# Optimization experiments

Hardware: AMD Instinct MI355X
Metric: run time of the kernel (lower is better)

## Reference

```python
import jax, jax.numpy as jnp
import numpy as np

BLOCK = 64
KH = 8        # num_k_head
G = 4         # gqa_group_size
D = 128       # model_hidden_size (head dim)
DG = 128      # gate_hidden_size
EPS = 1e-6
BSZ = 4
MAXS = 4096
LENGTHS = np.array([4096, 3584, 3072, 4096])


def rotate_half(x):
    h = x.shape[-1] // 2
    return jnp.concatenate([-x[..., h:], x[..., :h]], axis=-1)


def rmsnorm(x, w):
    x32 = x.astype(jnp.float32)
    y = x32 * jax.lax.rsqrt(jnp.mean(x32 * x32, axis=-1, keepdims=True) + EPS)
    return (y * w).astype(x.dtype)


def _rope_tables(n_pos, dim):
    inv = 1.0 / (10000.0 ** (np.arange(0, dim, 2, dtype=np.float32) / dim))
    ang = np.arange(n_pos, dtype=np.float32)[:, None] * inv[None, :]
    emb = np.concatenate([ang, ang], axis=-1)
    return np.cos(emb), np.sin(emb)


def setup_inputs() -> dict:
    key = jax.random.key(0)
    k1, k2, k3, k4, k5, k6 = jax.random.split(key, 6)
    total = int(LENGTHS.sum())
    cu = np.concatenate([[0], np.cumsum(LENGTHS)]).astype(np.int32)
    unpad_idx = np.concatenate([b * MAXS + np.arange(L) for b, L in enumerate(LENGTHS)]).astype(np.int64)
    # block-causal + validity mask (bool), shape (BSZ, 1, MAXS, MAXS//BLOCK)
    nb = MAXS // BLOCK
    qpos = np.arange(MAXS)
    bidx = np.arange(nb)
    causal = (qpos[:, None] // BLOCK) >= bidx[None, :]
    qvalid = qpos[None, :] < LENGTHS[:, None]
    bvalid = (bidx * BLOCK)[None, :] < LENGTHS[:, None]
    mask = causal[None] & qvalid[:, :, None] & bvalid[:, None, :]
    cos_q, sin_q = _rope_tables(MAXS, DG)
    cos_k, sin_k = _rope_tables(nb, DG)
    xavq = float(np.sqrt(6.0 / (D + DG)))
    xavk = float(np.sqrt(6.0 / (2 * D + DG)))
    return {
        "q": jax.random.normal(k1, (total, KH * G, D), jnp.float32),
        "k": jax.random.normal(k2, (total, KH, D), jnp.float32),
        "wq": jax.random.uniform(k3, (KH, G, D, DG), jnp.float32, -xavq, xavq),
        "wk": jax.random.uniform(k4, (KH, 2 * D, DG), jnp.float32, -xavk, xavk),
        "qnorm_w": jnp.ones((DG,), jnp.float32),
        "knorm_w": jnp.ones((DG,), jnp.float32),
        "cos_q": jnp.tile(jnp.asarray(cos_q)[None], (BSZ, 1, 1)),
        "sin_q": jnp.tile(jnp.asarray(sin_q)[None], (BSZ, 1, 1)),
        "cos_k": jnp.tile(jnp.asarray(cos_k)[None], (BSZ, 1, 1)),
        "sin_k": jnp.tile(jnp.asarray(sin_k)[None], (BSZ, 1, 1)),
        "attention_mask": jnp.asarray(mask)[:, None, :, :],
        "cu_seqlens": jnp.asarray(cu),
        "unpad_indices": jnp.asarray(unpad_idx),
        "max_seqlen": MAXS,
    }


def reference(q, k, wq, wk, qnorm_w, knorm_w, cos_q, sin_q, cos_k, sin_k,
              attention_mask, cu_seqlens, unpad_indices, max_seqlen):
    T = q.shape[0]
    bsz = cu_seqlens.shape[0] - 1
    nb = max_seqlen // BLOCK
    lengths = cu_seqlens[1:] - cu_seqlens[:-1]

    # --- Q path: per-group head-pooling projection (HeadPoolingLinear, Qproj) ---
    qp = jnp.einsum('skgi,kgio->sko', q.reshape(T, KH, G, D), wq)  # (T, KH, DG)
    qpad = jnp.zeros((bsz * max_seqlen, KH, DG), q.dtype).at[unpad_indices].set(qp)
    qpad = qpad.reshape(bsz, max_seqlen, KH, DG).transpose(0, 2, 1, 3)  # (b, KH, S, DG)
    qpad = rmsnorm(qpad, qnorm_w)
    qpad = qpad * cos_q[:, None] + rotate_half(qpad) * sin_q[:, None]

    # --- K path: pad, block max+avg pool (masked for varlen), project ---
    kpad = jnp.zeros((bsz * max_seqlen, KH, D), k.dtype).at[unpad_indices].set(k)
    kpad = kpad.reshape(bsz, nb, BLOCK, KH, D)
    pos = jnp.arange(max_seqlen).reshape(nb, BLOCK)
    valid = pos[None] < lengths[:, None, None]          # (b, nb, BLOCK)
    v = valid[..., None, None]                          # (b, nb, BLOCK, 1, 1)
    cnt = valid.sum(-1)[..., None, None]                # (b, nb, 1, 1)
    kmax = jnp.where(v, kpad, -jnp.inf).max(axis=2)
    kmax = jnp.where(cnt > 0, kmax, 0.0)
    kavg = jnp.where(v, kpad, 0.0).sum(axis=2) / jnp.maximum(cnt, 1).astype(k.dtype)
    kcat = jnp.concatenate([kmax, kavg], axis=-1)       # (b, nb, KH, 2D)
    kk = jnp.einsum('bhsi,hio->bhso', kcat.transpose(0, 2, 1, 3), wk)  # (b, KH, nb, DG)
    kk = rmsnorm(kk, knorm_w)
    kk = kk * cos_k[:, None] + rotate_half(kk) * sin_k[:, None]

    # --- QK gate scores ---
    attn = jnp.einsum('bhsd,bhtd->bhst', qpad, kk) * (1.0 / np.sqrt(DG))
    return jnp.where(attention_mask, attn, -1e20)
```

## Files before the change

### kernel.cpp

```cpp
#include <hip/hip_runtime.h>
#include <cstdint>
#include <cstddef>

#define BSZ   4
#define MAXS  4096
#define NB    64
#define KH    8
#define GQ    4
#define DH    128
#define DG    128
#define KHGD  4096
#define GD    512

__global__ __launch_bounds__(256, 2)
void qproj_kernel(const float* __restrict__ q,
                  const float* __restrict__ wq,
                  const float* __restrict__ qnw,
                  const float* __restrict__ cosq,
                  const float* __restrict__ sinq,
                  const int*   __restrict__ cu,
                  float* __restrict__ qr,
                  int T)
{
    __shared__ float At[64][68];
    __shared__ float Bt[64][128];

    const int tid = threadIdx.x;
    const int h   = blockIdx.y;
    const int t0  = blockIdx.x * 64;
    const int tr  = tid >> 4;
    const int tc  = tid & 15;

    float acc[4][8];
#pragma unroll
    for (int j = 0; j < 4; ++j)
#pragma unroll
        for (int i = 0; i < 8; ++i) acc[j][i] = 0.f;

    const float* qb = q  + (size_t)t0 * KHGD + (size_t)h * GD;
    const float* wb = wq + (size_t)h * GD * DG;

    const float* Ar  = &At[tr * 4][0];
    const float* Bp0 = &Bt[0][tc * 4];
    const float* Bp1 = &Bt[0][64 + tc * 4];

    for (int kc = 0; kc < 8; ++kc) {
        const int kb = kc * 64;
#pragma unroll
        for (int i = 0; i < 4; ++i) {
            const int fid = tid + i * 256;
            const int m = fid >> 4, c4 = (fid & 15) * 4;
            const int mg = (t0 + m < T) ? m : 0;
            const float4 v = *(const float4*)(qb + (size_t)mg * KHGD + kb + c4);
            *(float4*)&At[m][c4] = v;
        }
#pragma unroll
        for (int i = 0; i < 8; ++i) {
            const int fid = tid + i * 256;
            const int kk = fid >> 5, o4 = (fid & 31) * 4;
            const float4 v = *(const float4*)(wb + (size_t)(kb + kk) * DG + o4);
            *(float4*)&Bt[kk][o4] = v;
        }
        __syncthreads();

#pragma unroll 8
        for (int kk = 0; kk < 64; ++kk) {
            const float a0 = Ar[kk];
            const float a1 = Ar[68 + kk];
            const float a2 = Ar[136 + kk];
            const float a3 = Ar[204 + kk];
            const float4 b0 = *(const float4*)(Bp0 + kk * 128);
            const float4 b1 = *(const float4*)(Bp1 + kk * 128);
#define QROW(j, aj)                                                         \
            acc[j][0] += aj * b0.x; acc[j][1] += aj * b0.y;                 \
            acc[j][2] += aj * b0.z; acc[j][3] += aj * b0.w;                 \
            acc[j][4] += aj * b1.x; acc[j][5] += aj * b1.y;                 \
            acc[j][6] += aj * b1.z; acc[j][7] += aj * b1.w;
            QROW(0, a0) QROW(1, a1) QROW(2, a2) QROW(3, a3)
#undef QROW
        }
        __syncthreads();
    }

    const int cu1 = cu[1], cu2 = cu[2], cu3 = cu[3];
    const float4 w0 = *(const float4*)(qnw + tc * 4);
    const float4 w1 = *(const float4*)(qnw + 64 + tc * 4);

#pragma unroll
    for (int j = 0; j < 4; ++j) {
        const int t = t0 + tr * 4 + j;
        float ss = 0.f;
#pragma unroll
        for (int i = 0; i < 8; ++i) ss += acc[j][i] * acc[j][i];
        ss += __shfl_xor(ss, 1);
        ss += __shfl_xor(ss, 2);
        ss += __shfl_xor(ss, 4);
        ss += __shfl_xor(ss, 8);
        const float r = 1.0f / sqrtf(ss * (1.0f / 128.0f) + 1e-6f);

        if (t < T) {
            int b = 0;
            if (t >= cu1) b = 1;
            if (t >= cu2) b = 2;
            if (t >= cu3) b = 3;
            const int cub = (b == 0) ? 0 : ((b == 1) ? cu1 : ((b == 2) ? cu2 : cu3));
            const int s = t - cub;

            float y[8];
            y[0] = acc[j][0] * r * w0.x; y[1] = acc[j][1] * r * w0.y;
            y[2] = acc[j][2] * r * w0.z; y[3] = acc[j][3] * r * w0.w;
            y[4] = acc[j][4] * r * w1.x; y[5] = acc[j][5] * r * w1.y;
            y[6] = acc[j][6] * r * w1.z; y[7] = acc[j][7] * r * w1.w;

            const float* cb = cosq + ((size_t)b * MAXS + s) * DG;
            const float* sb = sinq + ((size_t)b * MAXS + s) * DG;
            const float4 c0 = *(const float4*)(cb + tc * 4);
            const float4 c1 = *(const float4*)(cb + 64 + tc * 4);
            const float4 s0v = *(const float4*)(sb + tc * 4);
            const float4 s1v = *(const float4*)(sb + 64 + tc * 4);

            float4 o0, o1;
            o0.x = y[0] * c0.x - y[4] * s0v.x;
            o0.y = y[1] * c0.y - y[5] * s0v.y;
            o0.z = y[2] * c0.z - y[6] * s0v.z;
            o0.w = y[3] * c0.w - y[7] * s0v.w;
            o1.x = y[4] * c1.x + y[0] * s1v.x;
            o1.y = y[5] * c1.y + y[1] * s1v.y;
            o1.z = y[6] * c1.z + y[2] * s1v.z;
            o1.w = y[7] * c1.w + y[3] * s1v.w;

            float* qrow = qr + (((size_t)b * KH + h) * MAXS + s) * DG;
            *(float4*)(qrow + tc * 4)      = o0;
            *(float4*)(qrow + 64 + tc * 4) = o1;
        }
    }
}

__global__ __launch_bounds__(256, 2)
void kproj_kernel(const float* __restrict__ k,
                  const float* __restrict__ wk,
                  const float* __restrict__ knw,
                  const float* __restrict__ cosk,
                  const float* __restrict__ sink,
                  const int*   __restrict__ cu,
                  float* __restrict__ krT)
{
    __shared__ float kcat[KH][2 * DH];

    const int tid = threadIdx.x;
    const int blk = blockIdx.x, b = blockIdx.y;
    const int lb = cu[b];
    const int L  = cu[b + 1] - lb;
    const int nv = min(64, L - blk * 64);
    if (nv <= 0) return;

    const float* kbase = k + (size_t)(lb + blk * 64) * (KH * DH) + tid * 4;
    float4 vmax = make_float4(-3.0e38f, -3.0e38f, -3.0e38f, -3.0e38f);
    float4 vsum = make_float4(0.f, 0.f, 0.f, 0.f);
#pragma unroll 4
    for (int j = 0; j < nv; ++j) {
        const float4 v = *(const float4*)(kbase + (size_t)j * (KH * DH));
        vmax.x = fmaxf(vmax.x, v.x); vmax.y = fmaxf(vmax.y, v.y);
        vmax.z = fmaxf(vmax.z, v.z); vmax.w = fmaxf(vmax.w, v.w);
        vsum.x += v.x; vsum.y += v.y; vsum.z += v.z; vsum.w += v.w;
    }
    {
        const float inv = 1.0f / (float)nv;
        const int hh = tid >> 5, dd = (tid & 31) * 4;
        *(float4*)&kcat[hh][dd] = vmax;
        const float4 va = make_float4(vsum.x * inv, vsum.y * inv, vsum.z * inv, vsum.w * inv);
        *(float4*)&kcat[hh][128 + dd] = va;
    }
    __syncthreads();

    const int h = tid >> 5, oc = tid & 31, o = oc * 4;
    float4 a4 = make_float4(0.f, 0.f, 0.f, 0.f);
    const float* wbb = wk + (size_t)h * (2 * DH) * DG + o;
#pragma unroll 8
    for (int kk = 0; kk < 2 * DH; ++kk) {
        const float a = kcat[h][kk];
        const float4 w = *(const float4*)(wbb + (size_t)kk * DG);
        a4.x += a * w.x; a4.y += a * w.y; a4.z += a * w.z; a4.w += a * w.w;
    }

    float ss = a4.x * a4.x + a4.y * a4.y + a4.z * a4.z + a4.w * a4.w;
    ss += __shfl_xor(ss, 1);
    ss += __shfl_xor(ss, 2);
    ss += __shfl_xor(ss, 4);
    ss += __shfl_xor(ss, 8);
    ss += __shfl_xor(ss, 16);
    const float r = 1.0f / sqrtf(ss * (1.0f / 128.0f) + 1e-6f);

    const float4 wn = *(const float4*)(knw + o);
    const float y0 = a4.x * r * wn.x;
    const float y1 = a4.y * r * wn.y;
    const float y2 = a4.z * r * wn.z;
    const float y3 = a4.w * r * wn.w;

    const float p0 = __shfl_xor(y0, 16);
    const float p1 = __shfl_xor(y1, 16);
    const float p2 = __shfl_xor(y2, 16);
    const float p3 = __shfl_xor(y3, 16);
    const float r0 = (oc < 16) ? -p0 : p0;
    const float r1 = (oc < 16) ? -p1 : p1;
    const float r2 = (oc < 16) ? -p2 : p2;
    const float r3 = (oc < 16) ? -p3 : p3;

    const float* cb = cosk + ((size_t)b * NB + blk) * DG + o;
    const float* sb = sink + ((size_t)b * NB + blk) * DG + o;
    const float4 c4 = *(const float4*)cb;
    const float4 s4 = *(const float4*)sb;

    float* ko = krT + (((size_t)b * KH + h) * DG + o) * NB + blk;
    ko[0 * NB] = y0 * c4.x + r0 * s4.x;
    ko[1 * NB] = y1 * c4.y + r1 * s4.y;
    ko[2 * NB] = y2 * c4.z + r2 * s4.z;
    ko[3 * NB] = y3 * c4.w + r3 * s4.w;
}

__global__ __launch_bounds__(256, 2)
void score_kernel(const float* __restrict__ qr,
                  const float* __restrict__ krT,
                  const int*   __restrict__ cu,
                  float* __restrict__ out)
{
    __shared__ float qtT[64][68];
    __shared__ float kt[128][64];

    const int tid = threadIdx.x;
    const int c = blockIdx.x, h = blockIdx.y, b = blockIdx.z;
    const int L  = cu[b + 1] - cu[b];
    const int s0 = c * 64;
    float* ob = out + (((size_t)b * KH + h) * MAXS + s0) * NB;

    if (s0 >= L) {
        const float4 m4 = make_float4(-1e20f, -1e20f, -1e20f, -1e20f);
#pragma unroll
        for (int i = 0; i < 4; ++i)
            *(float4*)(ob + (size_t)(tid + i * 256) * 4) = m4;
        return;
    }
    const int nt = c + 1;

    const float* ktg = krT + ((size_t)b * KH + h) * DG * NB;
#pragma unroll
    for (int i = 0; i < 8; ++i) {
        const int fid = tid + i * 256;
        const int o = fid >> 4, tp = (fid & 15) * 4;
        *(float4*)&kt[o][tp] = *(const float4*)(ktg + (size_t)o * NB + tp);
    }

    const int ts = tid & 15;
    const int tq = tid >> 4;
    float acc[4][4];
#pragma unroll
    for (int j = 0; j < 4; ++j)
#pragma unroll
        for (int i = 0; i < 4; ++i) acc[j][i] = 0.f;

    const float* qg = qr + (((size_t)b * KH + h) * MAXS + s0) * DG;

    for (int ko = 0; ko < 128; ko += 64) {
        __syncthreads();
#pragma unroll
        for (int i = 0; i < 4; ++i) {
            const int fid = tid + i * 256;
            const int m = fid >> 4, c4 = (fid & 15) * 4;
            const float4 v = *(const float4*)(qg + (size_t)m * DG + ko + c4);
            qtT[c4 + 0][m] = v.x;
            qtT[c4 + 1][m] = v.y;
            qtT[c4 + 2][m] = v.z;
            qtT[c4 + 3][m] = v.w;
        }
        __syncthreads();

        if (tq * 4 < nt) {
#pragma unroll 8
            for (int oo = 0; oo < 64; ++oo) {
                const float4 av = *(const float4*)&qtT[oo][ts * 4];
                const float4 bv = *(const float4*)&kt[ko + oo][tq * 4];
                acc[0][0] += av.x * bv.x; acc[0][1] += av.x * bv.y;
                acc[0][2] += av.x * bv.z; acc[0][3] += av.x * bv.w;
                acc[1][0] += av.y * bv.x; acc[1][1] += av.y * bv.y;
                acc[1][2] += av.y * bv.z; acc[1][3] += av.y * bv.w;
                acc[2][0] += av.z * bv.x; acc[2][1] += av.z * bv.y;
                acc[2][2] += av.z * bv.z; acc[2][3] += av.z * bv.w;
                acc[3][0] += av.w * bv.x; acc[3][1] += av.w * bv.y;
                acc[3][2] += av.w * bv.z; acc[3][3] += av.w * bv.w;
            }
        }
    }

    const float scale = 0.08838834764831845f;
#pragma unroll
    for (int j = 0; j < 4; ++j) {
        const int s = s0 + ts * 4 + j;
        const bool sv = (s < L);
        float4 v;
        v.x = (sv && (tq * 4 + 0) < nt) ? acc[j][0] * scale : -1e20f;
        v.y = (sv && (tq * 4 + 1) < nt) ? acc[j][1] * scale : -1e20f;
        v.z = (sv && (tq * 4 + 2) < nt) ? acc[j][2] * scale : -1e20f;
        v.w = (sv && (tq * 4 + 3) < nt) ? acc[j][3] * scale : -1e20f;
        *(float4*)(ob + (size_t)(ts * 4 + j) * NB + tq * 4) = v;
    }
}

extern "C" void kernel_launch(void* const* d_in, const int* in_sizes, int n_in,
                              void* d_out, int out_size, void* d_ws, size_t ws_size,
                              hipStream_t stream)
{
    const float* q    = (const float*)d_in[0];
    const float* k    = (const float*)d_in[1];
    const float* wq   = (const float*)d_in[2];
    const float* wk   = (const float*)d_in[3];
    const float* qnw  = (const float*)d_in[4];
    const float* knw  = (const float*)d_in[5];
    const float* cosq = (const float*)d_in[6];
    const float* sinq = (const float*)d_in[7];
    const float* cosk = (const float*)d_in[8];
    const float* sink = (const float*)d_in[9];
    const int* cu = (const int*)d_in[11];

    const int T = in_sizes[0] / KHGD;

    float* qr  = (float*)d_ws;
    float* krT = qr + (size_t)BSZ * KH * MAXS * DG;
    (void)ws_size; (void)n_in; (void)out_size;

    dim3 g1((T + 63) / 64, KH);
    qproj_kernel<<<g1, 256, 0, stream>>>(q, wq, qnw, cosq, sinq, cu, qr, T);
    kproj_kernel<<<dim3(NB, BSZ), 256, 0, stream>>>(k, wk, knw, cosk, sink, cu, krT);
    score_kernel<<<dim3(NB, KH, BSZ), 256, 0, stream>>>(qr, krT, cu, (float*)d_out);
}
```

Baseline: 588.9 us.

## Use split-bf16 MFMA for Q projection and score GEMMs

Replaces the scalar FP32 FMA GEMMs in the Q projection and score kernels with bf16 MFMA instructions. To keep accuracy close to FP32, each operand is split into hi and lo bf16 parts and three MFMAs are issued per tile. A new prep kernel repacks wq into an MFMA-friendly hi/lo layout on every call. Intermediate Q and K are stored as bf16 hi/lo pairs in an unpadded row layout. The trade-off is three times the matrix-core instructions plus conversion overhead, and some precision risk from dropping the lo*lo term.

Result: faster. 513.7 us (-12.8%).

```diff
diff --git a/kernel.cpp b/kernel.cpp
--- a/kernel.cpp
+++ b/kernel.cpp
@@ -6,132 +6,162 @@
 #define MAXS  4096
 #define NB    64
 #define KH    8
-#define GQ    4
 #define DH    128
 #define DG    128
 #define KHGD  4096
 #define GD    512
 
-__global__ __launch_bounds__(256, 2)
-void qproj_kernel(const float* __restrict__ q,
-                  const float* __restrict__ wq,
-                  const float* __restrict__ qnw,
-                  const float* __restrict__ cosq,
-                  const float* __restrict__ sinq,
-                  const int*   __restrict__ cu,
-                  float* __restrict__ qr,
-                  int T)
-{
-    __shared__ float At[64][68];
-    __shared__ float Bt[64][128];
-
-    const int tid = threadIdx.x;
-    const int h   = blockIdx.y;
-    const int t0  = blockIdx.x * 64;
-    const int tr  = tid >> 4;
-    const int tc  = tid & 15;
-
-    float acc[4][8];
-#pragma unroll
-    for (int j = 0; j < 4; ++j)
-#pragma unroll
-        for (int i = 0; i < 8; ++i) acc[j][i] = 0.f;
-
-    const float* qb = q  + (size_t)t0 * KHGD + (size_t)h * GD;
-    const float* wb = wq + (size_t)h * GD * DG;
-
-    const float* Ar  = &At[tr * 4][0];
-    const float* Bp0 = &Bt[0][tc * 4];
-    const float* Bp1 = &Bt[0][64 + tc * 4];
-
-    for (int kc = 0; kc < 8; ++kc) {
-        const int kb = kc * 64;
-#pragma unroll
-        for (int i = 0; i < 4; ++i) {
-            const int fid = tid + i * 256;
-            const int m = fid >> 4, c4 = (fid & 15) * 4;
-            const int mg = (t0 + m < T) ? m : 0;
-            const float4 v = *(const float4*)(qb + (size_t)mg * KHGD + kb + c4);
-            *(float4*)&At[m][c4] = v;
+typedef __attribute__((ext_vector_type(8))) short  short8;
+typedef __attribute__((ext_vector_type(4))) float  f32x4;
+
+static __device__ __forceinline__ unsigned bf16hi_bits(float x) {
+    unsigned u = __float_as_uint(x);
+    return (u + 0x7FFFu + ((u >> 16) & 1u)) & 0xFFFF0000u;
+}
+static __device__ __forceinline__ unsigned short bf16_rne(float x) {
+    unsigned u = __float_as_uint(x);
+    return (unsigned short)((u + 0x7FFFu + ((u >> 16) & 1u)) >> 16);
+}
+
+__global__ __launch_bounds__(256)
+void prep_wq(const float* __restrict__ wq, unsigned short* __restrict__ Bp)
+{
+    const int wid  = blockIdx.x * 4 + (threadIdx.x >> 6);
+    const int lane = threadIdx.x & 63;
+    const int h  = wid >> 7, kt = (wid >> 4) & 7, kf = (wid >> 3) & 1, cf = wid & 7;
+    const int n  = cf * 16 + (lane & 15);
+    const int k0 = kt * 64 + kf * 32 + (lane >> 4) * 8;
+
+    short8 hi, lo;
+#pragma unroll
+    for (int j = 0; j < 8; ++j) {
+        const float x = wq[(size_t)(h * GD + k0 + j) * DG + n];
+        const unsigned hb = bf16hi_bits(x);
+        hi[j] = (short)(hb >> 16);
+        lo[j] = (short)bf16_rne(x - __uint_as_float(hb));
+    }
+    unsigned short* p = Bp + (size_t)wid * 1024 + lane * 8;
+    *(short8*)p         = hi;
+    *(short8*)(p + 512) = lo;
+}
+
+__global__ __launch_bounds__(64, 2)
+void qproj_mfma(const float* __restrict__ q,
+                const unsigned short* __restrict__ Bp,
+                const float* __restrict__ qnw,
+                const float* __restrict__ cosq,
+                const float* __restrict__ sinq,
+                const int*   __restrict__ cu,
+                unsigned short* __restrict__ qh,
+                unsigned short* __restrict__ ql,
+                int T)
+{
+    const int lane = threadIdx.x;
+    const int h    = blockIdx.x;
+    const int row0 = blockIdx.y * 64;
+    const int lr = lane & 15, lq = lane >> 4;
+
+    f32x4 acc[4][8];
+#pragma unroll
+    for (int rf = 0; rf < 4; ++rf)
+#pragma unroll
+        for (int cf = 0; cf < 8; ++cf) acc[rf][cf] = (f32x4){0.f, 0.f, 0.f, 0.f};
+
+    const float* qb = q + (size_t)h * GD + lq * 8;
+    const float* aptr[4];
+#pragma unroll
+    for (int rf = 0; rf < 4; ++rf) {
+        int grow = row0 + rf * 16 + lr;
+        if (grow > T - 1) grow = T - 1;
+        aptr[rf] = qb + (size_t)grow * KHGD;
+    }
+
+    for (int kt = 0; kt < 8; ++kt) {
+        const int kb = kt * 64;
+#pragma unroll
+        for (int kf = 0; kf < 2; ++kf) {
+            f32x4 a0[4], a1[4];
+#pragma unroll
+            for (int rf = 0; rf < 4; ++rf) {
+                const float* p = aptr[rf] + kb + kf * 32;
+                a0[rf] = *(const f32x4*)p;
+                a1[rf] = *(const f32x4*)(p + 4);
+            }
+            short8 ah[4], al[4];
+#pragma unroll
+            for (int rf = 0; rf < 4; ++rf) {
+#pragma unroll
+                for (int j = 0; j < 4; ++j) {
+                    float x = a0[rf][j];
+                    unsigned hb = bf16hi_bits(x);
+                    ah[rf][j] = (short)(hb >> 16);
+                    al[rf][j] = (short)bf16_rne(x - __uint_as_float(hb));
+                    float y = a1[rf][j];
+                    unsigned hb2 = bf16hi_bits(y);
+                    ah[rf][j + 4] = (short)(hb2 >> 16);
+                    al[rf][j + 4] = (short)bf16_rne(y - __uint_as_float(hb2));
+                }
+            }
+            const unsigned short* bp =
+                Bp + (size_t)(((h * 8 + kt) * 2 + kf) * 8) * 1024 + lane * 8;
+#pragma unroll
+            for (int cf = 0; cf < 8; ++cf) {
+                const short8 bh = *(const short8*)(bp + cf * 1024);
+                const short8 bl = *(const short8*)(bp + cf * 1024 + 512);
+#pragma unroll
+                for (int rf = 0; rf < 4; ++rf) {
+                    acc[rf][cf] = __builtin_amdgcn_mfma_f32_16x16x32_bf16(ah[rf], bh, acc[rf][cf], 0, 0, 0);
+                    acc[rf][cf] = __builtin_amdgcn_mfma_f32_16x16x32_bf16(ah[rf], bl, acc[rf][cf], 0, 0, 0);
+                    acc[rf][cf] = __builtin_amdgcn_mfma_f32_16x16x32_bf16(al[rf], bh, acc[rf][cf], 0, 0, 0);
+                }
+            }
         }
-#pragma unroll
-        for (int i = 0; i < 8; ++i) {
-            const int fid = tid + i * 256;
-            const int kk = fid >> 5, o4 = (fid & 31) * 4;
-            const float4 v = *(const float4*)(wb + (size_t)(kb + kk) * DG + o4);
-            *(float4*)&Bt[kk][o4] = v;
-        }
-        __syncthreads();
-
-#pragma unroll 8
-        for (int kk = 0; kk < 64; ++kk) {
-            const float a0 = Ar[kk];
-            const float a1 = Ar[68 + kk];
-            const float a2 = Ar[136 + kk];
-            const float a3 = Ar[204 + kk];
-            const float4 b0 = *(const float4*)(Bp0 + kk * 128);
-            const float4 b1 = *(const float4*)(Bp1 + kk * 128);
-#define QROW(j, aj)                                                         \
-            acc[j][0] += aj * b0.x; acc[j][1] += aj * b0.y;                 \
-            acc[j][2] += aj * b0.z; acc[j][3] += aj * b0.w;                 \
-            acc[j][4] += aj * b1.x; acc[j][5] += aj * b1.y;                 \
-            acc[j][6] += aj * b1.z; acc[j][7] += aj * b1.w;
-            QROW(0, a0) QROW(1, a1) QROW(2, a2) QROW(3, a3)
-#undef QROW
-        }
-        __syncthreads();
     }
 
     const int cu1 = cu[1], cu2 = cu[2], cu3 = cu[3];
-    const float4 w0 = *(const float4*)(qnw + tc * 4);
-    const float4 w1 = *(const float4*)(qnw + 64 + tc * 4);
-
-#pragma unroll
-    for (int j = 0; j < 4; ++j) {
-        const int t = t0 + tr * 4 + j;
-        float ss = 0.f;
-#pragma unroll
-        for (int i = 0; i < 8; ++i) ss += acc[j][i] * acc[j][i];
-        ss += __shfl_xor(ss, 1);
-        ss += __shfl_xor(ss, 2);
-        ss += __shfl_xor(ss, 4);
-        ss += __shfl_xor(ss, 8);
-        const float r = 1.0f / sqrtf(ss * (1.0f / 128.0f) + 1e-6f);
-
-        if (t < T) {
-            int b = 0;
-            if (t >= cu1) b = 1;
-            if (t >= cu2) b = 2;
-            if (t >= cu3) b = 3;
-            const int cub = (b == 0) ? 0 : ((b == 1) ? cu1 : ((b == 2) ? cu2 : cu3));
-            const int s = t - cub;
-
-            float y[8];
-            y[0] = acc[j][0] * r * w0.x; y[1] = acc[j][1] * r * w0.y;
-            y[2] = acc[j][2] * r * w0.z; y[3] = acc[j][3] * r * w0.w;
-            y[4] = acc[j][4] * r * w1.x; y[5] = acc[j][5] * r * w1.y;
-            y[6] = acc[j][6] * r * w1.z; y[7] = acc[j][7] * r * w1.w;
-
-            const float* cb = cosq + ((size_t)b * MAXS + s) * DG;
-            const float* sb = sinq + ((size_t)b * MAXS + s) * DG;
-            const float4 c0 = *(const float4*)(cb + tc * 4);
-            const float4 c1 = *(const float4*)(cb + 64 + tc * 4);
-            const float4 s0v = *(const float4*)(sb + tc * 4);
-            const float4 s1v = *(const float4*)(sb + 64 + tc * 4);
-
-            float4 o0, o1;
-            o0.x = y[0] * c0.x - y[4] * s0v.x;
-            o0.y = y[1] * c0.y - y[5] * s0v.y;
-            o0.z = y[2] * c0.z - y[6] * s0v.z;
-            o0.w = y[3] * c0.w - y[7] * s0v.w;
-            o1.x = y[4] * c1.x + y[0] * s1v.x;
-            o1.y = y[5] * c1.y + y[1] * s1v.y;
-            o1.z = y[6] * c1.z + y[2] * s1v.z;
-            o1.w = y[7] * c1.w + y[3] * s1v.w;
-
-            float* qrow = qr + (((size_t)b * KH + h) * MAXS + s) * DG;
-            *(float4*)(qrow + tc * 4)      = o0;
-            *(float4*)(qrow + 64 + tc * 4) = o1;
+    float wn[8];
+#pragma unroll
+    for (int cf = 0; cf < 8; ++cf) wn[cf] = qnw[cf * 16 + lr];
+
+#pragma unroll
+    for (int rf = 0; rf < 4; ++rf) {
+#pragma unroll
+        for (int r = 0; r < 4; ++r) {
+            float vv[8];
+            float ss = 0.f;
+#pragma unroll
+            for (int cf = 0; cf < 8; ++cf) { vv[cf] = acc[rf][cf][r]; ss += vv[cf] * vv[cf]; }
+            ss += __shfl_xor(ss, 1);
+            ss += __shfl_xor(ss, 2);
+            ss += __shfl_xor(ss, 4);
+            ss += __shfl_xor(ss, 8);
+            const float rn = 1.0f / sqrtf(ss * (1.0f / 128.0f) + 1e-6f);
+
+            const int t = row0 + rf * 16 + lq * 4 + r;
+            if (t < T) {
+                int b = 0, cub = 0;
+                if (t >= cu1) { b = 1; cub = cu1; }
+                if (t >= cu2) { b = 2; cub = cu2; }
+                if (t >= cu3) { b = 3; cub = cu3; }
+                const int s = t - cub;
+
+                float y[8];
+#pragma unroll
+                for (int cf = 0; cf < 8; ++cf) y[cf] = vv[cf] * rn * wn[cf];
+
+                const float* cb = cosq + ((size_t)b * MAXS + s) * DG + lr;
+                const float* sb = sinq + ((size_t)b * MAXS + s) * DG + lr;
+                unsigned short* oh = qh + ((size_t)t * KH + h) * DG + lr;
+                unsigned short* ol = ql + ((size_t)t * KH + h) * DG + lr;
+#pragma unroll
+                for (int cf = 0; cf < 8; ++cf) {
+                    const float rot = (cf < 4) ? -y[cf + 4] : y[cf - 4];
+                    const float o = y[cf] * cb[cf * 16] + rot * sb[cf * 16];
+                    const unsigned hb = bf16hi_bits(o);
+                    oh[cf * 16] = (unsigned short)(hb >> 16);
+                    ol[cf * 16] = bf16_rne(o - __uint_as_float(hb));
+                }
+            }
         }
     }
 }
@@ -143,7 +173,8 @@
                   const float* __restrict__ cosk,
                   const float* __restrict__ sink,
                   const int*   __restrict__ cu,
-                  float* __restrict__ krT)
+                  unsigned short* __restrict__ krh,
+                  unsigned short* __restrict__ krl)
 {
     __shared__ float kcat[KH][2 * DH];
 
@@ -211,97 +242,86 @@
     const float4 c4 = *(const float4*)cb;
     const float4 s4 = *(const float4*)sb;
 
-    float* ko = krT + (((size_t)b * KH + h) * DG + o) * NB + blk;
-    ko[0 * NB] = y0 * c4.x + r0 * s4.x;
-    ko[1 * NB] = y1 * c4.y + r1 * s4.y;
-    ko[2 * NB] = y2 * c4.z + r2 * s4.z;
-    ko[3 * NB] = y3 * c4.w + r3 * s4.w;
+    float v[4];
+    v[0] = y0 * c4.x + r0 * s4.x;
+    v[1] = y1 * c4.y + r1 * s4.y;
+    v[2] = y2 * c4.z + r2 * s4.z;
+    v[3] = y3 * c4.w + r3 * s4.w;
+
+    ushort4 sh, sl;
+    unsigned hb;
+    hb = bf16hi_bits(v[0]); sh.x = (unsigned short)(hb >> 16); sl.x = bf16_rne(v[0] - __uint_as_float(hb));
+    hb = bf16hi_bits(v[1]); sh.y = (unsigned short)(hb >> 16); sl.y = bf16_rne(v[1] - __uint_as_float(hb));
+    hb = bf16hi_bits(v[2]); sh.z = (unsigned short)(hb >> 16); sl.z = bf16_rne(v[2] - __uint_as_float(hb));
+    hb = bf16hi_bits(v[3]); sh.w = (unsigned short)(hb >> 16); sl.w = bf16_rne(v[3] - __uint_as_float(hb));
+
+    const size_t ko = (((size_t)b * KH + h) * NB + blk) * DG + o;
+    *(ushort4*)(krh + ko) = sh;
+    *(ushort4*)(krl + ko) = sl;
 }
 
 __global__ __launch_bounds__(256, 2)
-void score_kernel(const float* __restrict__ qr,
-                  const float* __restrict__ krT,
-                  const int*   __restrict__ cu,
-                  float* __restrict__ out)
-{
-    __shared__ float qtT[64][68];
-    __shared__ float kt[128][64];
-
+void score_mfma(const unsigned short* __restrict__ qh,
+                const unsigned short* __restrict__ ql,
+                const unsigned short* __restrict__ krh,
+                const unsigned short* __restrict__ krl,
+                const int* __restrict__ cu,
+                float* __restrict__ out, int T)
+{
     const int tid = threadIdx.x;
+    const int lane = tid & 63, wid = tid >> 6;
     const int c = blockIdx.x, h = blockIdx.y, b = blockIdx.z;
-    const int L  = cu[b + 1] - cu[b];
-    const int s0 = c * 64;
-    float* ob = out + (((size_t)b * KH + h) * MAXS + s0) * NB;
-
-    if (s0 >= L) {
-        const float4 m4 = make_float4(-1e20f, -1e20f, -1e20f, -1e20f);
-#pragma unroll
-        for (int i = 0; i < 4; ++i)
-            *(float4*)(ob + (size_t)(tid + i * 256) * 4) = m4;
+    const int L = cu[b + 1] - cu[b];
+    float* ob = out + (((size_t)b * KH + h) * MAXS + c * 64) * NB;
+
+    if (c * 64 >= L) {
+        const f32x4 m4 = (f32x4){-1e20f, -1e20f, -1e20f, -1e20f};
+#pragma unroll
+        for (int i = 0; i < 4; ++i) ((f32x4*)ob)[tid + i * 256] = m4;
         return;
     }
-    const int nt = c + 1;
-
-    const float* ktg = krT + ((size_t)b * KH + h) * DG * NB;
-#pragma unroll
-    for (int i = 0; i < 8; ++i) {
-        const int fid = tid + i * 256;
-        const int o = fid >> 4, tp = (fid & 15) * 4;
-        *(float4*)&kt[o][tp] = *(const float4*)(ktg + (size_t)o * NB + tp);
-    }
-
-    const int ts = tid & 15;
-    const int tq = tid >> 4;
-    float acc[4][4];
-#pragma unroll
-    for (int j = 0; j < 4; ++j)
-#pragma unroll
-        for (int i = 0; i < 4; ++i) acc[j][i] = 0.f;
-
-    const float* qg = qr + (((size_t)b * KH + h) * MAXS + s0) * DG;
-
-    for (int ko = 0; ko < 128; ko += 64) {
-        __syncthreads();
-#pragma unroll
-        for (int i = 0; i < 4; ++i) {
-            const int fid = tid + i * 256;
-            const int m = fid >> 4, c4 = (fid & 15) * 4;
-            const float4 v = *(const float4*)(qg + (size_t)m * DG + ko + c4);
-            qtT[c4 + 0][m] = v.x;
-            qtT[c4 + 1][m] = v.y;
-            qtT[c4 + 2][m] = v.z;
-            qtT[c4 + 3][m] = v.w;
+    const int nt  = c + 1;
+    const int ncf = (nt + 15) >> 4;
+    const int lr = lane & 15, lq = lane >> 4;
+
+    int qrow = cu[b] + c * 64 + wid * 16 + lr;
+    if (qrow > T - 1) qrow = T - 1;
+    const unsigned short* qhp = qh + ((size_t)qrow * KH + h) * DG + lq * 8;
+    const unsigned short* qlp = ql + ((size_t)qrow * KH + h) * DG + lq * 8;
+    const unsigned short* kbh = krh + (((size_t)b * KH + h) * NB + lr) * DG + lq * 8;
+    const unsigned short* kbl = krl + (((size_t)b * KH + h) * NB + lr) * DG + lq * 8;
+
+    f32x4 acc[4];
+#pragma unroll
+    for (int cf = 0; cf < 4; ++cf) acc[cf] = (f32x4){0.f, 0.f, 0.f, 0.f};
+
+#pragma unroll
+    for (int kf = 0; kf < 4; ++kf) {
+        const short8 ah = *(const short8*)(qhp + kf * 32);
+        const short8 al = *(const short8*)(qlp + kf * 32);
+#pragma unroll
+        for (int cf = 0; cf < 4; ++cf) {
+            if (cf < ncf) {
+                const short8 bh = *(const short8*)(kbh + cf * 2048 + kf * 32);
+                const short8 bl = *(const short8*)(kbl + cf * 2048 + kf * 32);
+                acc[cf] = __builtin_amdgcn_mfma_f32_16x16x32_bf16(ah, bh, acc[cf], 0, 0, 0);
+                acc[cf] = __builtin_amdgcn_mfma_f32_16x16x32_bf16(ah, bl, acc[cf], 0, 0, 0);
+                acc[cf] = __builtin_amdgcn_mfma_f32_16x16x32_bf16(al, bh, acc[cf], 0, 0, 0);
+            }
         }
-        __syncthreads();
-
-        if (tq * 4 < nt) {
-#pragma unroll 8
-            for (int oo = 0; oo < 64; ++oo) {
-                const float4 av = *(const float4*)&qtT[oo][ts * 4];
-                const float4 bv = *(const float4*)&kt[ko + oo][tq * 4];
-                acc[0][0] += av.x * bv.x; acc[0][1] += av.x * bv.y;
-                acc[0][2] += av.x * bv.z; acc[0][3] += av.x * bv.w;
-                acc[1][0] += av.y * bv.x; acc[1][1] += av.y * bv.y;
-                acc[1][2] += av.y * bv.z; acc[1][3] += av.y * bv.w;
-                acc[2][0] += av.z * bv.x; acc[2][1] += av.z * bv.y;
-                acc[2][2] += av.z * bv.z; acc[2][3] += av.z * bv.w;
-                acc[3][0] += av.w * bv.x; acc[3][1] += av.w * bv.y;
-                acc[3][2] += av.w * bv.z; acc[3][3] += av.w * bv.w;
-            }
+    }
+
+    const float scale = 0.08838834764831845f;
+#pragma unroll
+    for (int cf = 0; cf < 4; ++cf) {
+        const int t = cf * 16 + lr;
+#pragma unroll
+        for (int r = 0; r < 4; ++r) {
+            const int srow = c * 64 + wid * 16 + lq * 4 + r;
+            float v = (cf < ncf) ? acc[cf][r] * scale : -1e20f;
+            v = (srow < L && t < nt) ? v : -1e20f;
+            ob[(size_t)(wid * 16 + lq * 4 + r) * NB + t] = v;
         }
-    }
-
-    const float scale = 0.08838834764831845f;
-#pragma unroll
-    for (int j = 0; j < 4; ++j) {
-        const int s = s0 + ts * 4 + j;
-        const bool sv = (s < L);
-        float4 v;
-        v.x = (sv && (tq * 4 + 0) < nt) ? acc[j][0] * scale : -1e20f;
-        v.y = (sv && (tq * 4 + 1) < nt) ? acc[j][1] * scale : -1e20f;
-        v.z = (sv && (tq * 4 + 2) < nt) ? acc[j][2] * scale : -1e20f;
-        v.w = (sv && (tq * 4 + 3) < nt) ? acc[j][3] * scale : -1e20f;
-        *(float4*)(ob + (size_t)(ts * 4 + j) * NB + tq * 4) = v;
     }
 }
 
@@ -319,16 +339,19 @@
     const float* sinq = (const float*)d_in[7];
     const float* cosk = (const float*)d_in[8];
     const float* sink = (const float*)d_in[9];
-    const int* cu = (const int*)d_in[11];
+    const int*   cu   = (const int*)d_in[11];
 
     const int T = in_sizes[0] / KHGD;
 
-    float* qr  = (float*)d_ws;
-    float* krT = qr + (size_t)BSZ * KH * MAXS * DG;
+    unsigned short* qh  = (unsigned short*)d_ws;
+    unsigned short* ql  = qh  + (size_t)T * KH * DG;
+    unsigned short* krh = ql  + (size_t)T * KH * DG;
+    unsigned short* krl = krh + (size_t)BSZ * KH * NB * DG;
+    unsigned short* Bp  = krl + (size_t)BSZ * KH * NB * DG;
     (void)ws_size; (void)n_in; (void)out_size;
 
-    dim3 g1((T + 63) / 64, KH);
-    qproj_kernel<<<g1, 256, 0, stream>>>(q, wq, qnw, cosq, sinq, cu, qr, T);
-    kproj_kernel<<<dim3(NB, BSZ), 256, 0, stream>>>(k, wk, knw, cosk, sink, cu, krT);
-    score_kernel<<<dim3(NB, KH, BSZ), 256, 0, stream>>>(qr, krT, cu, (float*)d_out);
-}
+    prep_wq<<<256, 256, 0, stream>>>(wq, Bp);
+    kproj_kernel<<<dim3(NB, BSZ), 256, 0, stream>>>(k, wk, knw, cosk, sink, cu, krh, krl);
+    qproj_mfma<<<dim3(KH, (T + 63) / 64), 64, 0, stream>>>(q, Bp, qnw, cosq, sinq, cu, qh, ql, T);
+    score_mfma<<<dim3(NB, KH, BSZ), 256, 0, stream>>>(qh, ql, krh, krl, cu, (float*)d_out, T);
+}
```
